# Kernel optimization log

Hardware: AMD Instinct MI355X
Metric: run time of the kernel (lower is better)

## Reference

```python
import jax, jax.numpy as jnp
import numpy as np
from jax import lax

SCALE = 2
NUM_POINTS = 4

def conv2d(x, w, b, pad):
    # x: [B,C,H,W], w: [O,I,kh,kw]
    y = lax.conv_general_dilated(x, w, (1, 1), [(pad, pad), (pad, pad)],
                                 dimension_numbers=("NCHW", "OIHW", "NCHW"))
    return y + b[None, :, None, None]

def grid_sample_border(feat, grid):
    # feat: [B,C,H,W]; grid: [B,Hg,Wg,2] in [-1,1] (x,y), align_corners=False,
    # padding_mode='border' (coordinates clipped before interpolation, as in torch).
    B, C, H, W = feat.shape
    Hg, Wg = grid.shape[1], grid.shape[2]
    gx = jnp.clip((grid[..., 0] + 1.0) * W / 2.0 - 0.5, 0.0, W - 1.0)
    gy = jnp.clip((grid[..., 1] + 1.0) * H / 2.0 - 0.5, 0.0, H - 1.0)
    x0 = jnp.floor(gx); y0 = jnp.floor(gy)
    fx = (gx - x0).reshape(B, 1, -1)
    fy = (gy - y0).reshape(B, 1, -1)
    x0i = jnp.clip(x0.astype(jnp.int32), 0, W - 1)
    y0i = jnp.clip(y0.astype(jnp.int32), 0, H - 1)
    x1i = jnp.clip(x0i + 1, 0, W - 1)
    y1i = jnp.clip(y0i + 1, 0, H - 1)
    featf = feat.reshape(B, C, H * W)
    def gather(yi, xi):
        idx = (yi * W + xi).reshape(B, 1, -1)
        return jnp.take_along_axis(featf, idx, axis=2)  # [B,C,Hg*Wg]
    v00 = gather(y0i, x0i); v01 = gather(y0i, x1i)
    v10 = gather(y1i, x0i); v11 = gather(y1i, x1i)
    out = (v00 * (1 - fx) * (1 - fy) + v01 * fx * (1 - fy)
           + v10 * (1 - fx) * fy + v11 * fx * fy)
    return out.reshape(B, C, Hg, Wg)

def setup_inputs() -> dict:
    key = jax.random.key(0)
    ks = jax.random.split(key, 8)
    B, Cin, Cout, H, W = 8, 256, 256, 64, 64
    high_feat = jax.random.normal(ks[0], (B, Cin, H, W), jnp.float32)
    low_feat = jax.random.normal(ks[1], (B, Cout, H * SCALE, W * SCALE), jnp.float32)
    W1 = jax.random.normal(ks[2], (Cin, Cin + Cout, 1, 1), jnp.float32) * 0.02
    b1 = jnp.zeros((Cin,), jnp.float32)
    # original inits offset_conv2 to zeros; use small random to exercise deformable sampling
    W2 = jax.random.normal(ks[3], (NUM_POINTS * 2, Cin, 3, 3), jnp.float32) * 0.01
    b2 = jnp.zeros((NUM_POINTS * 2,), jnp.float32)
    Wf = jax.random.normal(ks[4], (Cout, Cin, 1, 1), jnp.float32) * 0.05
    bf = jnp.zeros((Cout,), jnp.float32)
    return {"high_feat": high_feat, "low_feat": low_feat, "W1": W1, "b1": b1,
            "W2": W2, "b2": b2, "Wf": Wf, "bf": bf}

def reference(high_feat, low_feat, W1, b1, W2, b2, Wf, bf):
    B, Cin, H, W = high_feat.shape
    H_up, W_up = H * SCALE, W * SCALE
    # bilinear upsample, align_corners=False (half-pixel centers)
    up_high = jax.image.resize(high_feat, (B, Cin, H_up, W_up), method="bilinear")
    concat = jnp.concatenate([up_high, low_feat], axis=1)
    off_feat = jax.nn.relu(conv2d(concat, W1, b1, 0))
    offsets = conv2d(off_feat, W2, b2, 1)  # [B, 2P, H_up, W_up]
    proc = conv2d(high_feat, Wf, bf, 0)    # [B, Cout, H, W]
    # base grid in [-1,1], (x,y)
    gy = jnp.linspace(-1.0, 1.0, H_up)
    gx = jnp.linspace(-1.0, 1.0, W_up)
    base = jnp.stack(jnp.meshgrid(gx, gy, indexing="xy"), axis=-1)  # [H_up,W_up,2]
    # offsets -> [B,P,2,H,W] -> [P,B,H,W,2], normalized to [-1,1] units
    off = offsets.reshape(B, NUM_POINTS, 2, H_up, W_up).transpose(1, 0, 3, 4, 2)
    norm = jnp.array([W_up, H_up], jnp.float32)
    off = off / norm * 2.0
    grids = base[None, None] + off  # [P,B,H_up,W_up,2]
    sampled = jax.vmap(lambda g: grid_sample_border(proc, g))(grids)  # [P,B,C,H_up,W_up]
    return jnp.mean(sampled, axis=0)
```

## Files before the change

kernel.cpp:

```cpp
#include <hip/hip_runtime.h>
#include <stdint.h>

#define NB   8
#define CH   256
#define HW0  4096
#define HW2  16384

typedef __attribute__((ext_vector_type(8))) short short8;
typedef __attribute__((ext_vector_type(8))) unsigned short u16x8;
typedef __attribute__((ext_vector_type(4))) unsigned short u16x4;
typedef __attribute__((ext_vector_type(4))) float floatx4;

__device__ inline unsigned short f2bf(float f) {
    union { float f; uint32_t u; } v; v.f = f;
    return (unsigned short)((v.u + 0x7FFFu + ((v.u >> 16) & 1u)) >> 16);
}
__device__ inline float bf2f(unsigned short h) {
    union { uint32_t u; float f; } v; v.u = ((uint32_t)h) << 16;
    return v.f;
}

__global__ __launch_bounds__(256) void ktrans(const float* __restrict__ src,
        unsigned short* __restrict__ dst, int M) {
    const int b = blockIdx.z, k0 = blockIdx.y * 32, m0 = blockIdx.x * 128;
    const int tid = threadIdx.x;
    __shared__ unsigned short tile[32][132];
    const float* s = src + ((size_t)b * CH + k0) * M + m0;
    for (int c = tid; c < 1024; c += 256) {
        int kk = c >> 5, mm = (c & 31) * 4;
        float4 v = *(const float4*)(s + (size_t)kk * M + mm);
        u16x4 o = { f2bf(v.x), f2bf(v.y), f2bf(v.z), f2bf(v.w) };
        *(u16x4*)&tile[kk][mm] = o;
    }
    __syncthreads();
    unsigned short* d = dst + ((size_t)b * M + m0) * CH + k0;
    for (int c = tid; c < 512; c += 256) {
        int mm = c >> 2, kc = (c & 3) * 8;
        u16x8 v;
        #pragma unroll
        for (int i = 0; i < 8; ++i) v[i] = tile[kc + i][mm];
        *(u16x8*)(d + (size_t)mm * CH + kc) = v;
    }
}

__global__ __launch_bounds__(256) void kwconv(const float* __restrict__ W1,
        const float* __restrict__ Wf, unsigned short* __restrict__ A1,
        unsigned short* __restrict__ A2) {
    int i = blockIdx.x * 256 + threadIdx.x;
    if (i < 512 * 256) {
        int n = i >> 8, k = i & 255;
        float v = (n < 256) ? W1[n * 512 + k] : Wf[(size_t)(n - 256) * 256 + k];
        A1[i] = f2bf(v);
    }
    if (i < 256 * 256) {
        int n = i >> 8, k = i & 255;
        A2[i] = f2bf(W1[n * 512 + 256 + k]);
    }
}

__global__ __launch_bounds__(256) void kwpack(const float* __restrict__ W2v,
        unsigned short* __restrict__ W3p) {
    int i = blockIdx.x * 256 + threadIdx.x;
    if (i >= 9 * 16 * 256) return;
    int ci = i & 255, o = (i >> 8) & 15, t = i >> 12;
    float v = (o < 8) ? W2v[((size_t)o * 256 + ci) * 9 + t] : 0.0f;
    W3p[i] = f2bf(v);
}

__global__ __launch_bounds__(256) void k1_mfma(
    const unsigned short* __restrict__ highT,
    const unsigned short* __restrict__ A1,
    const float* __restrict__ bfv,
    float* __restrict__ T, float* __restrict__ procT)
{
    const int b = blockIdx.z;
    const int m0 = blockIdx.x * 128;
    const int n0 = blockIdx.y * 128;
    const int tid = threadIdx.x;
    __shared__ __attribute__((aligned(16))) unsigned short smem[2 * 128 * 40];
    unsigned short* As = smem;
    unsigned short* Xs = smem + 128 * 40;
    const int lane = tid & 63, wid = tid >> 6;
    const int wn = (wid >> 1) * 64, wm = (wid & 1) * 64;
    const int l15 = lane & 15, quad = lane >> 4;

    floatx4 acc[4][4];
    #pragma unroll
    for (int i = 0; i < 4; ++i)
        #pragma unroll
        for (int j = 0; j < 4; ++j)
            acc[i][j] = (floatx4){0.f, 0.f, 0.f, 0.f};

    const unsigned short* Xg = highT + ((size_t)b * HW0 + m0) * CH;

    for (int k0 = 0; k0 < 256; k0 += 32) {
        for (int c = tid; c < 512; c += 256) {
            int row = c >> 2, kc = (c & 3) * 8;
            *(u16x8*)&As[row * 40 + kc] =
                *(const u16x8*)(A1 + (size_t)(n0 + row) * CH + k0 + kc);
            *(u16x8*)&Xs[row * 40 + kc] =
                *(const u16x8*)(Xg + (size_t)row * CH + k0 + kc);
        }
        __syncthreads();
        short8 af[4], bfr[4];
        #pragma unroll
        for (int i = 0; i < 4; ++i)
            af[i] = *(const short8*)&As[(wn + i * 16 + l15) * 40 + quad * 8];
        #pragma unroll
        for (int j = 0; j < 4; ++j)
            bfr[j] = *(const short8*)&Xs[(wm + j * 16 + l15) * 40 + quad * 8];
        #pragma unroll
        for (int i = 0; i < 4; ++i)
            #pragma unroll
            for (int j = 0; j < 4; ++j)
                acc[i][j] = __builtin_amdgcn_mfma_f32_16x16x32_bf16(
                    af[i], bfr[j], acc[i][j], 0, 0, 0);
        __syncthreads();
    }

    if (n0 < 256) {
        #pragma unroll
        for (int i = 0; i < 4; ++i) {
            int nb = n0 + wn + i * 16 + quad * 4;
            #pragma unroll
            for (int r = 0; r < 4; ++r) {
                int n = nb + r;
                #pragma unroll
                for (int j = 0; j < 4; ++j) {
                    int m = m0 + wm + j * 16 + l15;
                    T[((size_t)b * CH + n) * HW0 + m] = acc[i][j][r];
                }
            }
        }
    } else {
        float* tf = (float*)smem;
        const int nc = n0 - 256;
        #pragma unroll
        for (int mq = 0; mq < 4; ++mq) {
            __syncthreads();
            if ((wid & 1) == (mq >> 1)) {
                #pragma unroll
                for (int jj = 0; jj < 2; ++jj) {
                    int j = (mq & 1) * 2 + jj;
                    int ml = j * 16 + l15 - (mq & 1) * 32;
                    #pragma unroll
                    for (int i = 0; i < 4; ++i) {
                        int nl = wn + i * 16 + quad * 4;
                        #pragma unroll
                        for (int r = 0; r < 4; ++r)
                            tf[ml * 132 + nl + r] = acc[i][j][r] + bfv[nc + nl + r];
                    }
                }
            }
            __syncthreads();
            int mm = tid >> 3;
            int c8 = tid & 7;
            float* dst = procT + ((size_t)b * HW0 + m0 + mq * 32 + mm) * CH + nc;
            #pragma unroll
            for (int k = 0; k < 4; ++k) {
                int col = c8 * 4 + k * 32;
                *(float4*)(dst + col) = *(const float4*)&tf[mm * 132 + col];
            }
        }
    }
}

__global__ __launch_bounds__(256) void k2_mfma(
    const unsigned short* __restrict__ lowT,
    const unsigned short* __restrict__ A2,
    const float* __restrict__ b1, const float* __restrict__ T,
    unsigned short* __restrict__ off_featT)
{
    const int b = blockIdx.z;
    const int m0 = blockIdx.x * 128;
    const int n0 = blockIdx.y * 128;
    const int tid = threadIdx.x;
    __shared__ unsigned short smem[2 * 128 * 40];
    unsigned short* As = smem;
    unsigned short* Xs = smem + 128 * 40;
    const int lane = tid & 63, wid = tid >> 6;
    const int wn = (wid >> 1) * 64, wm = (wid & 1) * 64;
    const int l15 = lane & 15, quad = lane >> 4;

    floatx4 acc[4][4];
    #pragma unroll
    for (int i = 0; i < 4; ++i)
        #pragma unroll
        for (int j = 0; j < 4; ++j)
            acc[i][j] = (floatx4){0.f, 0.f, 0.f, 0.f};

    const unsigned short* Xg = lowT + ((size_t)b * HW2 + m0) * CH;

    for (int k0 = 0; k0 < 256; k0 += 32) {
        for (int c = tid; c < 512; c += 256) {
            int row = c >> 2, kc = (c & 3) * 8;
            *(u16x8*)&As[row * 40 + kc] =
                *(const u16x8*)(A2 + (size_t)(n0 + row) * CH + k0 + kc);
            *(u16x8*)&Xs[row * 40 + kc] =
                *(const u16x8*)(Xg + (size_t)row * CH + k0 + kc);
        }
        __syncthreads();
        short8 af[4], bfr[4];
        #pragma unroll
        for (int i = 0; i < 4; ++i)
            af[i] = *(const short8*)&As[(wn + i * 16 + l15) * 40 + quad * 8];
        #pragma unroll
        for (int j = 0; j < 4; ++j)
            bfr[j] = *(const short8*)&Xs[(wm + j * 16 + l15) * 40 + quad * 8];
        #pragma unroll
        for (int i = 0; i < 4; ++i)
            #pragma unroll
            for (int j = 0; j < 4; ++j)
                acc[i][j] = __builtin_amdgcn_mfma_f32_16x16x32_bf16(
                    af[i], bfr[j], acc[i][j], 0, 0, 0);
        __syncthreads();
    }

    const int y = blockIdx.x;
    int hk = y >> 1;
    int yA, yB; float wyA, wyB;
    if (y & 1) { yA = hk; yB = min(hk + 1, 63); wyA = 0.75f; wyB = 0.25f; }
    else       { yB = hk; yA = max(hk - 1, 0);  wyA = 0.25f; wyB = 0.75f; }

    int xA[4], xB[4]; float wxA[4], wxB[4];
    #pragma unroll
    for (int j = 0; j < 4; ++j) {
        int x = wm + j * 16 + l15;
        int xk = x >> 1;
        if (x & 1) { xA[j] = xk; xB[j] = min(xk + 1, 63); wxA[j] = 0.75f; wxB[j] = 0.25f; }
        else       { xB[j] = xk; xA[j] = max(xk - 1, 0);  wxA[j] = 0.25f; wxB[j] = 0.75f; }
    }

    #pragma unroll
    for (int i = 0; i < 4; ++i) {
        int nb = n0 + wn + i * 16 + quad * 4;
        #pragma unroll
        for (int r = 0; r < 4; ++r) {
            int n = nb + r;
            const float* tb  = T + ((size_t)b * CH + n) * HW0;
            const float* trA = tb + yA * 64;
            const float* trB = tb + yB * 64;
            float bias = b1[n];
            #pragma unroll
            for (int j = 0; j < 4; ++j) {
                float up = wyA * (wxA[j] * trA[xA[j]] + wxB[j] * trA[xB[j]])
                         + wyB * (wxA[j] * trB[xA[j]] + wxB[j] * trB[xB[j]]);
                acc[i][j][r] = fmaxf(acc[i][j][r] + up + bias, 0.0f);
            }
        }
    }

    unsigned short (*tile)[136] = (unsigned short (*)[136])smem;
    for (int xh = 0; xh < 2; ++xh) {
        __syncthreads();
        if ((wid & 1) == xh) {
            #pragma unroll
            for (int i = 0; i < 4; ++i) {
                int nc = wn + i * 16 + quad * 4;
                #pragma unroll
                for (int j = 0; j < 4; ++j) {
                    int xr = j * 16 + l15;
                    unsigned int lo = (unsigned int)f2bf(acc[i][j][0])
                                    | ((unsigned int)f2bf(acc[i][j][1]) << 16);
                    unsigned int hi = (unsigned int)f2bf(acc[i][j][2])
                                    | ((unsigned int)f2bf(acc[i][j][3]) << 16);
                    *(unsigned int*)&tile[xr][nc]     = lo;
                    *(unsigned int*)&tile[xr][nc + 2] = hi;
                }
            }
        }
        __syncthreads();
        for (int c = tid; c < 1024; c += 256) {
            int xr = c >> 4, nc = (c & 15) * 8;
            u16x8 v = *(u16x8*)&tile[xr][nc];
            *(u16x8*)(off_featT +
                ((size_t)b * HW2 + (size_t)y * 128 + xh * 64 + xr) * CH + n0 + nc) = v;
        }
    }
}

__global__ __launch_bounds__(256) void k3_mfma(
    const unsigned short* __restrict__ offT,
    const unsigned short* __restrict__ W3p,
    float* __restrict__ offs)
{
    const int b = blockIdx.y;
    const int y = blockIdx.x;
    const int tid = threadIdx.x;
    const int lane = tid & 63, w = tid >> 6;
    const int l15 = lane & 15, quad = lane >> 4;

    floatx4 acc[2];
    acc[0] = (floatx4){0.f, 0.f, 0.f, 0.f};
    acc[1] = (floatx4){0.f, 0.f, 0.f, 0.f};

    const unsigned short* xb = offT + (size_t)b * HW2 * CH;
    const int xbase = w * 32 + l15;

    for (int k0 = 0; k0 < 256; k0 += 32) {
        #pragma unroll
        for (int t = 0; t < 9; ++t) {
            const int dy = t / 3 - 1, dx = t % 3 - 1;
            const int yy = y + dy;
            if ((unsigned)yy >= 128u) continue;
            short8 bw = *(const short8*)(W3p + (size_t)(t * 16 + l15) * CH
                                         + k0 + quad * 8);
            const unsigned short* rowp = xb + ((size_t)yy * 128) * CH + k0 + quad * 8;
            #pragma unroll
            for (int j = 0; j < 2; ++j) {
                int xx = xbase + j * 16 + dx;
                short8 ax = (short8){0, 0, 0, 0, 0, 0, 0, 0};
                if ((unsigned)xx < 128u)
                    ax = *(const short8*)(rowp + (size_t)xx * CH);
                acc[j] = __builtin_amdgcn_mfma_f32_16x16x32_bf16(
                    ax, bw, acc[j], 0, 0, 0);
            }
        }
    }

    if (l15 < 8) {
        float* ob = offs + ((size_t)b * 8 + l15) * HW2 + (size_t)y * 128;
        #pragma unroll
        for (int j = 0; j < 2; ++j) {
            int xpix = w * 32 + j * 16 + quad * 4;
            *(floatx4*)(ob + xpix) = acc[j];
        }
    }
}

__global__ __launch_bounds__(256) void k4_sample(
    const float* __restrict__ offs, const float* __restrict__ b2v,
    const float* __restrict__ procT, float* __restrict__ out)
{
    const int blk = blockIdx.x;
    const int b  = blk & 7;
    const int r  = blk >> 3;
    const int y  = r >> 1;
    const int xt = r & 1;
    const int tid = threadIdx.x;
    const int lane = tid & 63, w = tid >> 6;

    __shared__ float4 sp[4][64];
    __shared__ float tile[4][16 * 65];

    if (tid < 64) {
        int x = xt * 64 + tid;
        float gxb = (2.0f * x) / 127.0f - 1.0f;
        float gyb = (2.0f * y) / 127.0f - 1.0f;
        const float* ob = offs + (size_t)b * 8 * HW2 + y * 128 + x;
        #pragma unroll
        for (int p = 0; p < 4; ++p) {
            float ox = ob[(2 * p) * HW2] + b2v[2 * p];
            float oy = ob[(2 * p + 1) * HW2] + b2v[2 * p + 1];
            float gx = gxb + ox * (2.0f / 128.0f);
            float gy = gyb + oy * (2.0f / 128.0f);
            float gxp = fminf(fmaxf((gx + 1.0f) * 32.0f - 0.5f, 0.0f), 63.0f);
            float gyp = fminf(fmaxf((gy + 1.0f) * 32.0f - 0.5f, 0.0f), 63.0f);
            float x0f = floorf(gxp), y0f = floorf(gyp);
            int x0 = (int)x0f, y0 = (int)y0f;
            int idx = (y0 * 64 + x0) * 256;
            int dxo = (x0 < 63) ? 256 : 0;
            int dyo = (y0 < 63) ? 16384 : 0;
            sp[p][tid] = make_float4(__int_as_float(idx),
                                     __int_as_float(dxo | (dyo << 16)),
                                     gxp - x0f, gyp - y0f);
        }
    }
    __syncthreads();

    const float* P = procT + (size_t)b * HW0 * CH + w * 64 + lane;
    float* tw = &tile[w][0];
    float* outb = out + ((size_t)b * CH + w * 64) * HW2 + (size_t)y * 128 + xt * 64;

    for (int chunk = 0; chunk < 4; ++chunk) {
        float a[16];
        #pragma unroll
        for (int i = 0; i < 16; ++i) a[i] = 0.f;
        #pragma unroll
        for (int i = 0; i < 16; ++i) {
            int px = chunk * 16 + i;
            #pragma unroll
            for (int p = 0; p < 4; ++p) {
                float4 s = sp[p][px];
                int idx  = __float_as_int(s.x);
                int pack = __float_as_int(s.y);
                int dxo = pack & 0xFFFF, dyo = pack >> 16;
                const float* q = P + idx;
                float v00 = q[0];
                float v01 = q[dxo];
                float v10 = q[dyo];
                float v11 = q[dyo + dxo];
                float top = v00 + s.z * (v01 - v00);
                float bot = v10 + s.z * (v11 - v10);
                a[i] += top + s.w * (bot - top);
            }
        }
        #pragma unroll
        for (int i = 0; i < 16; ++i) tw[i * 65 + lane] = a[i] * 0.25f;
        #pragma unroll
        for (int g = 0; g < 16; ++g) {
            int c   = g * 4 + (lane >> 4);
            int pxl = lane & 15;
            outb[(size_t)c * HW2 + chunk * 16 + pxl] = tw[pxl * 65 + c];
        }
    }
}

extern "C" void kernel_launch(void* const* d_in, const int* in_sizes, int n_in,
                              void* d_out, int out_size, void* d_ws, size_t ws_size,
                              hipStream_t stream) {
    const float* high = (const float*)d_in[0];
    const float* low  = (const float*)d_in[1];
    const float* W1   = (const float*)d_in[2];
    const float* b1   = (const float*)d_in[3];
    const float* W2v  = (const float*)d_in[4];
    const float* b2v  = (const float*)d_in[5];
    const float* Wf   = (const float*)d_in[6];
    const float* bfv  = (const float*)d_in[7];
    float* out = (float*)d_out;
    float* ws  = (float*)d_ws;

    float* T     = ws;
    float* procT = ws + 8388608;
    float* offs  = ws + 16777216;
    unsigned short* highT = (unsigned short*)(ws + 17825792);
    unsigned short* A1 = highT + 8388608;
    unsigned short* A2 = A1 + 131072;

    unsigned short* W3p = highT;

    unsigned short* lowT      = (unsigned short*)out;
    unsigned short* off_featT = ((unsigned short*)out) + 33554432;

    ktrans<<<dim3(32, 8, NB), 256, 0, stream>>>(high, highT, HW0);
    ktrans<<<dim3(128, 8, NB), 256, 0, stream>>>(low, lowT, HW2);
    kwconv<<<dim3(512), 256, 0, stream>>>(W1, Wf, A1, A2);

    k1_mfma<<<dim3(32, 4, NB), 256, 0, stream>>>(highT, A1, bfv, T, procT);
    kwpack<<<dim3(144), 256, 0, stream>>>(W2v, W3p);
    k2_mfma<<<dim3(128, 2, NB), 256, 0, stream>>>(lowT, A2, b1, T, off_featT);
    k3_mfma<<<dim3(128, NB), 256, 0, stream>>>(off_featT, W3p, offs);
    k4_sample<<<dim3(2048), 256, 0, stream>>>(offs, b2v, procT, out);
}
```

Baseline: 551.0 us.

## Vectorize sampling gathers with float4 channel loads and precomputed bilinear weights

Reassigns work in the sampling kernel so each lane handles four consecutive channels and each wave handles its own pixels. This replaces scalar gathers with float4 gathers from the channel-last proc tensor. Bilinear corner weights, including the 1/4 mean factor, are precomputed once per point in shared memory, so the inner loop becomes plain FMAs instead of lerps. The transpose tile is re-laid out for the new mapping and adds two block barriers per chunk. Output stores now cover 8 pixels per channel row instead of 16, which makes the write segments shorter.

```diff
diff --git a/kernel.cpp b/kernel.cpp
--- a/kernel.cpp
+++ b/kernel.cpp
@@ -336,15 +336,16 @@
     const int b  = blk & 7;
     const int r  = blk >> 3;
     const int y  = r >> 1;
-    const int xt = r & 1;
+    const int xh = r & 1;
     const int tid = threadIdx.x;
     const int lane = tid & 63, w = tid >> 6;
 
-    __shared__ float4 sp[4][64];
-    __shared__ float tile[4][16 * 65];
+    __shared__ int2   sp_i[4][64];
+    __shared__ float4 sp_w[4][64];
+    __shared__ float  tile[4][8 * 260];
 
     if (tid < 64) {
-        int x = xt * 64 + tid;
+        int x = xh * 64 + tid;
         float gxb = (2.0f * x) / 127.0f - 1.0f;
         float gyb = (2.0f * y) / 127.0f - 1.0f;
         const float* ob = offs + (size_t)b * 8 * HW2 + y * 128 + x;
@@ -361,48 +362,49 @@
             int idx = (y0 * 64 + x0) * 256;
             int dxo = (x0 < 63) ? 256 : 0;
             int dyo = (y0 < 63) ? 16384 : 0;
-            sp[p][tid] = make_float4(__int_as_float(idx),
-                                     __int_as_float(dxo | (dyo << 16)),
-                                     gxp - x0f, gyp - y0f);
+            float fx = gxp - x0f, fy = gyp - y0f;
+            float ex = 1.0f - fx, ey = 1.0f - fy;
+            sp_i[p][tid] = make_int2(idx, dxo | (dyo << 16));
+            sp_w[p][tid] = make_float4(0.25f * ex * ey, 0.25f * fx * ey,
+                                       0.25f * ex * fy, 0.25f * fx * fy);
         }
     }
     __syncthreads();
 
-    const float* P = procT + (size_t)b * HW0 * CH + w * 64 + lane;
+    const float* P = procT + (size_t)b * HW0 * CH + lane * 4;
     float* tw = &tile[w][0];
-    float* outb = out + ((size_t)b * CH + w * 64) * HW2 + (size_t)y * 128 + xt * 64;
-
-    for (int chunk = 0; chunk < 4; ++chunk) {
-        float a[16];
-        #pragma unroll
-        for (int i = 0; i < 16; ++i) a[i] = 0.f;
-        #pragma unroll
-        for (int i = 0; i < 16; ++i) {
-            int px = chunk * 16 + i;
+    float* outb = out + (size_t)b * CH * HW2 + (size_t)y * 128 + xh * 64 + w * 16;
+
+    for (int c8 = 0; c8 < 2; ++c8) {
+        #pragma unroll
+        for (int i = 0; i < 8; ++i) {
+            int lpx = w * 16 + c8 * 8 + i;
+            float4 a = make_float4(0.f, 0.f, 0.f, 0.f);
             #pragma unroll
             for (int p = 0; p < 4; ++p) {
-                float4 s = sp[p][px];
-                int idx  = __float_as_int(s.x);
-                int pack = __float_as_int(s.y);
-                int dxo = pack & 0xFFFF, dyo = pack >> 16;
-                const float* q = P + idx;
-                float v00 = q[0];
-                float v01 = q[dxo];
-                float v10 = q[dyo];
-                float v11 = q[dyo + dxo];
-                float top = v00 + s.z * (v01 - v00);
-                float bot = v10 + s.z * (v11 - v10);
-                a[i] += top + s.w * (bot - top);
-            }
-        }
-        #pragma unroll
-        for (int i = 0; i < 16; ++i) tw[i * 65 + lane] = a[i] * 0.25f;
-        #pragma unroll
-        for (int g = 0; g < 16; ++g) {
-            int c   = g * 4 + (lane >> 4);
-            int pxl = lane & 15;
-            outb[(size_t)c * HW2 + chunk * 16 + pxl] = tw[pxl * 65 + c];
-        }
+                int2 si = sp_i[p][lpx];
+                float4 sw = sp_w[p][lpx];
+                int dxo = si.y & 0xFFFF, dyo = si.y >> 16;
+                const float* q = P + si.x;
+                float4 v00 = *(const float4*)(q);
+                float4 v01 = *(const float4*)(q + dxo);
+                float4 v10 = *(const float4*)(q + dyo);
+                float4 v11 = *(const float4*)(q + dyo + dxo);
+                a.x += sw.x * v00.x + sw.y * v01.x + sw.z * v10.x + sw.w * v11.x;
+                a.y += sw.x * v00.y + sw.y * v01.y + sw.z * v10.y + sw.w * v11.y;
+                a.z += sw.x * v00.z + sw.y * v01.z + sw.z * v10.z + sw.w * v11.z;
+                a.w += sw.x * v00.w + sw.y * v01.w + sw.z * v10.w + sw.w * v11.w;
+            }
+            *(float4*)&tw[i * 260 + lane * 4] = a;
+        }
+        __syncthreads();
+        #pragma unroll
+        for (int g = 0; g < 32; ++g) {
+            int c   = g * 8 + (lane >> 3);
+            int pxl = lane & 7;
+            outb[(size_t)c * HW2 + c8 * 8 + pxl] = tw[pxl * 260 + c];
+        }
+        __syncthreads();
     }
 }
 
```

After: 540.2 us. 1.02x faster.
